# Optimization experiments

Measured on AMD Instinct MI355X. Metric: run time of the kernel, lower is better.

The kernel has to match this reference:

```python
import jax, jax.numpy as jnp
import numpy as np

CH = 256
GROUPS = 8
EPS = 1e-5


def setup_inputs() -> dict:
    key = jax.random.key(0)
    ks = jax.random.split(key, 10)
    c = CH
    s = 1.0 / np.sqrt(c)
    return {
        "x": jax.random.normal(ks[0], (4, c, 64, 64), dtype=jnp.float32),
        "gn_gamma": jnp.ones((c,), jnp.float32),
        "gn_beta": jnp.zeros((c,), jnp.float32),
        "wq": jax.random.normal(ks[1], (c, c), jnp.float32) * s,
        "bq": jnp.zeros((c,), jnp.float32),
        "wk": jax.random.normal(ks[2], (c, c), jnp.float32) * s,
        "bk": jnp.zeros((c,), jnp.float32),
        "wv": jax.random.normal(ks[3], (c, c), jnp.float32) * s,
        "bv": jnp.zeros((c,), jnp.float32),
        "wp": jax.random.normal(ks[4], (c, c), jnp.float32) * s,
        "bp": jnp.zeros((c,), jnp.float32),
    }


def group_norm(x, gamma, beta):
    b, c, h, w = x.shape
    g = GROUPS
    xg = x.reshape(b, g, c // g, h, w)
    mu = jnp.mean(xg, axis=(2, 3, 4), keepdims=True)
    var = jnp.var(xg, axis=(2, 3, 4), keepdims=True)
    xn = ((xg - mu) * jax.lax.rsqrt(var + EPS)).reshape(b, c, h, w)
    return xn * gamma[None, :, None, None] + beta[None, :, None, None]


def reference(x, gn_gamma, gn_beta, wq, bq, wk, bk, wv, bv, wp, bp):
    b, c, h, w = x.shape
    xn = group_norm(x, gn_gamma, gn_beta).reshape(b, c, h * w)  # [b,c,n]
    # 1x1 conv == channel matmul: out[b,o,n] = sum_c w[o,c] x[b,c,n] + bias
    q = jnp.einsum('oc,bcn->bon', wq, xn) + bq[None, :, None]
    k = jnp.einsum('oc,bcn->bon', wk, xn) + bk[None, :, None]
    v = jnp.einsum('oc,bcn->bon', wv, xn) + bv[None, :, None]
    scores = jnp.einsum('bcn,bcm->bnm', q, k) / jnp.sqrt(jnp.float32(c))
    attn = jax.nn.softmax(scores, axis=-1)  # [b,n,m]
    out = jnp.einsum('bnm,bcm->bcn', attn, v)
    out = jnp.einsum('oc,bcn->bon', wp, out) + bp[None, :, None]
    return out.reshape(b, c, h, w) + x
```

## Files before the change

### kernel.cpp

```cpp
#include <hip/hip_runtime.h>
#include <stdint.h>

#define BB 4
#define CC 256
#define NN 4096
#define GG 8

typedef unsigned short u16;
typedef __attribute__((ext_vector_type(4))) float f32x4;
typedef __attribute__((ext_vector_type(16))) float f32x16;
typedef __attribute__((ext_vector_type(8))) short s16x8;
typedef __attribute__((ext_vector_type(4))) u16 u16x4;
typedef __attribute__((ext_vector_type(8))) u16 u16x8;

__device__ __forceinline__ u16 f2bf(float f) {
  union { float f; uint32_t u; } v; v.f = f;
  return (u16)((v.u + 0x7FFFu + ((v.u >> 16) & 1u)) >> 16);
}
__device__ __forceinline__ float bf2f(uint32_t u) {
  union { uint32_t u; float f; } v; v.u = u << 16;
  return v.f;
}

__device__ __forceinline__ void async16(const void* g, void* l) {
  __builtin_amdgcn_global_load_lds(
      (const __attribute__((address_space(1))) void*)g,
      (__attribute__((address_space(3))) void*)l, 16, 0, 0);
}

__global__ __launch_bounds__(256) void wcvt_kernel(
    const float* __restrict__ w0, const float* __restrict__ w1,
    const float* __restrict__ w2, const float* __restrict__ w3,
    u16* __restrict__ dst) {
  const float* src = (blockIdx.y == 0) ? w0 : (blockIdx.y == 1) ? w1
                   : (blockIdx.y == 2) ? w2 : w3;
  int i = blockIdx.x * 256 + threadIdx.x;
  f32x4 v = ((const f32x4*)src)[i];
  u16x4 o;
  o[0] = f2bf(v[0]); o[1] = f2bf(v[1]); o[2] = f2bf(v[2]); o[3] = f2bf(v[3]);
  ((u16x4*)(dst + (size_t)blockIdx.y * 65536))[i] = o;
}

__global__ __launch_bounds__(256) void gn_part_kernel(
    const float* __restrict__ x, float* __restrict__ part) {
  int bg = blockIdx.x, seg = blockIdx.y;
  const f32x4* xp = (const f32x4*)(x + (size_t)bg * 131072 + seg * 16384);
  float s = 0.f, ss = 0.f;
  for (int i = threadIdx.x; i < 4096; i += 256) {
    f32x4 v = xp[i];
    s += v[0] + v[1] + v[2] + v[3];
    ss += v[0]*v[0] + v[1]*v[1] + v[2]*v[2] + v[3]*v[3];
  }
  for (int d = 1; d < 64; d <<= 1) {
    s += __shfl_xor(s, d, 64);
    ss += __shfl_xor(ss, d, 64);
  }
  __shared__ float red[8];
  int w = threadIdx.x >> 6, lane = threadIdx.x & 63;
  if (lane == 0) { red[w*2] = s; red[w*2+1] = ss; }
  __syncthreads();
  if (threadIdx.x == 0) {
    part[(bg*8 + seg)*2]     = red[0]+red[2]+red[4]+red[6];
    part[(bg*8 + seg)*2 + 1] = red[1]+red[3]+red[5]+red[7];
  }
}

__global__ __launch_bounds__(512) void gnqkv_kernel(
    const float* __restrict__ x, const float* __restrict__ part,
    const float* __restrict__ gamma, const float* __restrict__ beta,
    const u16* __restrict__ wbf,
    const float* __restrict__ bq, const float* __restrict__ bk,
    const float* __restrict__ bv,
    u16* __restrict__ Qtm, u16* __restrict__ Ktm, u16* __restrict__ Vcm) {
  __shared__ float gstat[16];
  __shared__ char t1[32768];
  __shared__ char t2[32768];
  const int b = blockIdx.y, n0 = blockIdx.x * 64, t = threadIdx.x;
  if (t < 8) {
    float S = 0.f, SS = 0.f;
    for (int seg = 0; seg < 8; ++seg) {
      S  += part[((b*8 + t)*8 + seg)*2];
      SS += part[((b*8 + t)*8 + seg)*2 + 1];
    }
    float mean = S * (1.0f/131072.0f);
    float var = SS * (1.0f/131072.0f) - mean*mean;
    gstat[t*2] = mean;
    gstat[t*2+1] = rsqrtf(var + 1e-5f);
  }
  __syncthreads();
  for (int p = 0; p < 8; ++p) {
    int c = p*32 + (t >> 4);
    int n4 = (t & 15) * 4;
    f32x4 v = *(const f32x4*)(x + ((size_t)b*CC + c)*NN + n0 + n4);
    float mean = gstat[(c>>5)*2], rstd = gstat[(c>>5)*2+1];
    float ga = gamma[c] * rstd;
    float be = beta[c] - mean * ga;
    u16x4 o;
    o[0]=f2bf(v[0]*ga+be); o[1]=f2bf(v[1]*ga+be);
    o[2]=f2bf(v[2]*ga+be); o[3]=f2bf(v[3]*ga+be);
    int swz = (((c & 7) ^ ((c >> 3) & 7)) << 4);
    *(u16x4*)(t1 + c*128 + ((n4*2) ^ swz)) = o;
  }
  __syncthreads();
  for (int p = 0; p < 4; ++p) {
    int n = p*16 + (t >> 5);
    int c0 = (t & 31) * 8;
    u16x8 o;
#pragma unroll
    for (int j = 0; j < 8; ++j) {
      int c = c0 + j;
      int swz = (((c & 7) ^ ((c >> 3) & 7)) << 4);
      o[j] = *(const u16*)(t1 + c*128 + ((n*2) ^ swz));
    }
    *(u16x8*)(t2 + n*512 + ((c0*2) ^ ((n & 7) << 4))) = o;
  }
  __syncthreads();
  const int lane = t & 63, w = t >> 6;
  const int wn = w >> 2, wo = w & 3;
  const int hi = lane >> 4, lo = lane & 15;
#pragma unroll
  for (int mat = 0; mat < 3; ++mat) {
    const u16* wm = wbf + mat*65536;
    f32x4 acc[2][4] = {};
    for (int kc = 0; kc < 8; ++kc) {
      s16x8 xf[2];
#pragma unroll
      for (int nf = 0; nf < 2; ++nf) {
        int n = wn*32 + nf*16 + lo;
        xf[nf] = *(const s16x8*)(t2 + n*512 + ((kc*64 + hi*16) ^ ((n & 7) << 4)));
      }
#pragma unroll
      for (int of = 0; of < 4; ++of) {
        int o = wo*64 + of*16 + lo;
        s16x8 wf = *(const s16x8*)(wm + (size_t)o*256 + kc*32 + hi*8);
        if (mat < 2) {
          acc[0][of] = __builtin_amdgcn_mfma_f32_16x16x32_bf16(xf[0], wf, acc[0][of], 0, 0, 0);
          acc[1][of] = __builtin_amdgcn_mfma_f32_16x16x32_bf16(xf[1], wf, acc[1][of], 0, 0, 0);
        } else {
          acc[0][of] = __builtin_amdgcn_mfma_f32_16x16x32_bf16(wf, xf[0], acc[0][of], 0, 0, 0);
          acc[1][of] = __builtin_amdgcn_mfma_f32_16x16x32_bf16(wf, xf[1], acc[1][of], 0, 0, 0);
        }
      }
    }
    if (mat < 2) {
      u16* Y = (mat == 0) ? Qtm : Ktm;
      const float* bias = (mat == 0) ? bq : bk;
#pragma unroll
      for (int nf = 0; nf < 2; ++nf)
#pragma unroll
        for (int of = 0; of < 4; ++of) {
          int oc = wo*64 + of*16 + lo;
          float bvv = bias[oc];
#pragma unroll
          for (int r = 0; r < 4; ++r) {
            int n = n0 + wn*32 + nf*16 + hi*4 + r;
            Y[((size_t)b*NN + n)*CC + oc] = f2bf(acc[nf][of][r] + bvv);
          }
        }
    } else {
#pragma unroll
      for (int nf = 0; nf < 2; ++nf)
#pragma unroll
        for (int of = 0; of < 4; ++of)
#pragma unroll
          for (int r = 0; r < 4; ++r) {
            int oc = wo*64 + of*16 + hi*4 + r;
            int n = n0 + wn*32 + nf*16 + lo;
            Vcm[((size_t)b*CC + oc)*NN + n] = f2bf(acc[nf][of][r] + bv[oc]);
          }
    }
  }
}

__global__ __launch_bounds__(256, 2) void flash_kernel(
    const u16* __restrict__ Q, const u16* __restrict__ K,
    const u16* __restrict__ V, uint32_t* __restrict__ Op32,
    float* __restrict__ Lpart) {
  __shared__ char kl[2][16384];
  __shared__ char vl[2][16384];
  const int bid = blockIdx.x;
  const int b    = bid & 3;
  const int part = ((bid >> 2) & 1) | (((bid >> 8) & 1) << 1);
  const int qb   = (bid >> 3) & 31;
  const int tid = threadIdx.x;
  const int lane = tid & 63;
  const int w = tid >> 6;
  const int cl = lane & 31;
  const int h = lane >> 5;
  const int q = qb*128 + w*32 + cl;

  s16x8 qreg[16];
  {
    const u16* qp = Q + ((size_t)b*NN + q)*CC + h*8;
#pragma unroll
    for (int kc = 0; kc < 16; ++kc) qreg[kc] = *(const s16x8*)(qp + kc*16);
  }
  f32x16 oacc[8];
#pragma unroll
  for (int i = 0; i < 8; ++i) oacc[i] = (f32x16)0.f;
  float Lp = 0.f;

  const char* kbase = (const char*)(K + (size_t)b*NN*CC);
  const char* vbase = (const char*)(V + (size_t)b*CC*NN);
  const int mbase = part*1024;

  auto stage = [&](int buf, int m0) {
#pragma unroll
    for (int p = 0; p < 4; ++p)
      async16(kbase + (size_t)(m0 + (tid & 31))*512 + ((tid >> 5) + p*8)*16,
              kl[buf] + p*4096 + tid*16);
#pragma unroll
    for (int p = 0; p < 4; ++p)
      async16(vbase + (size_t)tid*8192 + (size_t)m0*2 + p*16,
              vl[buf] + p*4096 + tid*16);
  };

  stage(0, mbase);
  stage(1, mbase + 32);

  const float SC = 0.0901684857f;

  for (int it = 0; it < 32; ++it) {
    const int cur = it & 1;
    if (it == 31) asm volatile("s_waitcnt vmcnt(0)" ::: "memory");
    else          asm volatile("s_waitcnt vmcnt(8)" ::: "memory");
    __builtin_amdgcn_s_barrier();
    asm volatile("" ::: "memory");

    f32x16 s0 = (f32x16)0.f;
    __builtin_amdgcn_s_setprio(1);
#pragma unroll
    for (int kc = 0; kc < 16; ++kc) {
      s16x8 kf = *(const s16x8*)(kl[cur] + (kc*2 + h)*512 + cl*16);
      s0 = __builtin_amdgcn_mfma_f32_32x32x16_bf16(kf, qreg[kc], s0, 0, 0, 0);
    }
    __builtin_amdgcn_s_setprio(0);

    s16x8 pf[2];
#pragma unroll
    for (int half = 0; half < 2; ++half) {
      float pe[8];
#pragma unroll
      for (int j = 0; j < 8; ++j) {
        float p = exp2f(s0[half*8 + j] * SC);
        pe[j] = p;
        Lp += p;
      }
      uint32_t a0, a1, a2, a3;
      asm("v_cvt_pk_bf16_f32 %0, %1, %2" : "=v"(a0) : "v"(pe[0]), "v"(pe[1]));
      asm("v_cvt_pk_bf16_f32 %0, %1, %2" : "=v"(a1) : "v"(pe[2]), "v"(pe[3]));
      asm("v_cvt_pk_bf16_f32 %0, %1, %2" : "=v"(a2) : "v"(pe[4]), "v"(pe[5]));
      asm("v_cvt_pk_bf16_f32 %0, %1, %2" : "=v"(a3) : "v"(pe[6]), "v"(pe[7]));
      asm("v_permlane32_swap_b32 %0, %1" : "+v"(a0), "+v"(a2));
      asm("v_permlane32_swap_b32 %0, %1" : "+v"(a1), "+v"(a3));
      union { uint32_t w[4]; s16x8 v; } u;
      u.w[0] = a0; u.w[1] = a1; u.w[2] = a2; u.w[3] = a3;
      pf[half] = u.v;
    }

    __builtin_amdgcn_s_setprio(1);
#pragma unroll
    for (int ks = 0; ks < 2; ++ks) {
#pragma unroll
      for (int ct = 0; ct < 8; ++ct) {
        s16x8 vf = *(const s16x8*)(vl[cur] + (ks*2 + h)*4096 + (ct*32 + cl)*16);
        oacc[ct] = __builtin_amdgcn_mfma_f32_32x32x16_bf16(vf, pf[ks], oacc[ct], 0, 0, 0);
      }
    }
    __builtin_amdgcn_s_setprio(0);
    __builtin_amdgcn_s_barrier();
    if (it < 30) stage(cur, mbase + (it + 2)*32);
  }

  float Lq = Lp + __shfl_xor(Lp, 32, 64);
  const int pb = part*4 + b;
  if (lane < 32) Lpart[(size_t)pb*NN + q] = Lq;
  const size_t basePB = (size_t)pb * 128 * NN;
#pragma unroll
  for (int ct = 0; ct < 8; ++ct) {
#pragma unroll
    for (int i2 = 0; i2 < 8; ++i2) {
      const int i = i2*2;
      float lo_ = oacc[ct][i], hi_ = oacc[ct][i+1];
      uint32_t pk;
      asm("v_cvt_pk_bf16_f32 %0, %1, %2" : "=v"(pk) : "v"(lo_), "v"(hi_));
      const int cp = ct*16 + ((i&3)>>1) + 4*(i>>2) + 2*h;
      Op32[basePB + (size_t)cp*NN + q] = pk;
    }
  }
}

__global__ __launch_bounds__(512) void proj_kernel(
    const uint32_t* __restrict__ Op32, const float* __restrict__ Lpart,
    const u16* __restrict__ wp, const float* __restrict__ bp,
    const float* __restrict__ resid, float* __restrict__ out) {
  __shared__ char t2[32768];
  const int b = blockIdx.y, m0 = blockIdx.x * 64, t = threadIdx.x;
  {
    const int q = m0 + (t & 63);
    const int m = t & 63;
    const int cg = t >> 6;
    float L = 0.f;
#pragma unroll
    for (int p = 0; p < 4; ++p) L += Lpart[(size_t)(p*4 + b)*NN + q];
    const float inv = 1.0f / L;
#pragma unroll
    for (int i = 0; i < 16; ++i) {
      const int cp = cg*16 + i;
      float v0 = 0.f, v1 = 0.f;
#pragma unroll
      for (int p = 0; p < 4; ++p) {
        uint32_t pk = Op32[(size_t)(p*4 + b)*128*NN + (size_t)cp*NN + q];
        v0 += bf2f(pk & 0xffffu);
        v1 += bf2f(pk >> 16);
      }
      v0 *= inv; v1 *= inv;
      uint32_t opk;
      asm("v_cvt_pk_bf16_f32 %0, %1, %2" : "=v"(opk) : "v"(v0), "v"(v1));
      *(uint32_t*)(t2 + m*512 + ((cp*4) ^ ((m & 7) << 4))) = opk;
    }
  }
  __syncthreads();
  const int lane = t & 63, w = t >> 6;
  const int wm = w >> 2, wo = w & 3;
  const int hi = lane >> 4, lo = lane & 15;
  f32x4 acc[2][4] = {};
  for (int kc = 0; kc < 8; ++kc) {
    s16x8 xf[2];
#pragma unroll
    for (int mf = 0; mf < 2; ++mf) {
      int m = wm*32 + mf*16 + lo;
      xf[mf] = *(const s16x8*)(t2 + m*512 + ((kc*64 + hi*16) ^ ((m & 7) << 4)));
    }
#pragma unroll
    for (int of = 0; of < 4; ++of) {
      int o = wo*64 + of*16 + lo;
      s16x8 wf = *(const s16x8*)(wp + (size_t)o*256 + kc*32 + hi*8);
      acc[0][of] = __builtin_amdgcn_mfma_f32_16x16x32_bf16(wf, xf[0], acc[0][of], 0, 0, 0);
      acc[1][of] = __builtin_amdgcn_mfma_f32_16x16x32_bf16(wf, xf[1], acc[1][of], 0, 0, 0);
    }
  }
#pragma unroll
  for (int mf = 0; mf < 2; ++mf)
#pragma unroll
    for (int of = 0; of < 4; ++of) {
      int oc0 = wo*64 + of*16 + hi*4;
#pragma unroll
      for (int r = 0; r < 4; ++r) {
        int m = m0 + wm*32 + mf*16 + lo;
        size_t idx = ((size_t)b*CC + oc0 + r)*NN + m;
        out[idx] = acc[mf][of][r] + bp[oc0 + r] + resid[idx];
      }
    }
}

extern "C" void kernel_launch(void* const* d_in, const int* in_sizes, int n_in,
                              void* d_out, int out_size, void* d_ws, size_t ws_size,
                              hipStream_t stream) {
  const float* x  = (const float*)d_in[0];
  const float* gg = (const float*)d_in[1];
  const float* gb = (const float*)d_in[2];
  const float* wq = (const float*)d_in[3];
  const float* bq = (const float*)d_in[4];
  const float* wk = (const float*)d_in[5];
  const float* bk = (const float*)d_in[6];
  const float* wv = (const float*)d_in[7];
  const float* bv = (const float*)d_in[8];
  const float* wp = (const float*)d_in[9];
  const float* bp = (const float*)d_in[10];
  float* out = (float*)d_out;

  char* ws = (char*)d_ws;
  const size_t MATS = (size_t)BB * NN * CC;
  u16* wbf  = (u16*)ws;
  u16* Qtm  = (u16*)(ws + (512 << 10));
  u16* Ktm  = Qtm + MATS;
  u16* Vcm  = Ktm + MATS;
  uint32_t* Op32 = (uint32_t*)(Vcm + MATS);
  float* Lpart   = (float*)(Op32 + (size_t)16*128*NN);
  float* part    = Lpart + (size_t)16*NN;

  wcvt_kernel<<<dim3(64, 4), 256, 0, stream>>>(wq, wk, wv, wp, wbf);
  gn_part_kernel<<<dim3(32, 8), 256, 0, stream>>>(x, part);
  gnqkv_kernel<<<dim3(64, 4), 512, 0, stream>>>(x, part, gg, gb, wbf,
                                                bq, bk, bv, Qtm, Ktm, Vcm);
  flash_kernel<<<512, 256, 0, stream>>>(Qtm, Ktm, Vcm, Op32, Lpart);
  proj_kernel<<<dim3(64, 4), 512, 0, stream>>>(Op32, Lpart, wbf + 3*65536,
                                               bp, x, out);
}
```

Before: 159.0 us.

## Split flash kernel waves into QK/softmax producers and PV consumers via LDS

The flash attention kernel now specializes its waves. Half compute QK^T scores and exponentials and write bf16 probabilities to a double-buffered LDS area. The other half consume them one step later for the PV MFMAs, so the two phases overlap across waves. The key split drops from four partitions to two, which halves partial outputs and the reduction work in proj_kernel. Each block covers 64 queries with dynamic LDS raised to 72KB, and exp2f is replaced with raw v_exp_f32. The larger LDS footprint may cut occupancy, and the producer/consumer barriers add sync cost per step.

```diff
diff --git a/kernel.cpp b/kernel.cpp
--- a/kernel.cpp
+++ b/kernel.cpp
@@ -176,21 +176,25 @@
     const u16* __restrict__ Q, const u16* __restrict__ K,
     const u16* __restrict__ V, uint32_t* __restrict__ Op32,
     float* __restrict__ Lpart) {
-  __shared__ char kl[2][16384];
-  __shared__ char vl[2][16384];
+  extern __shared__ char smem[];
+  char* kl = smem;
+  char* vl = smem + 32768;
+  char* pl = smem + 65536;
   const int bid = blockIdx.x;
   const int b    = bid & 3;
-  const int part = ((bid >> 2) & 1) | (((bid >> 8) & 1) << 1);
-  const int qb   = (bid >> 3) & 31;
+  const int part = (bid >> 2) & 1;
+  const int qb   = bid >> 3;
   const int tid = threadIdx.x;
   const int lane = tid & 63;
   const int w = tid >> 6;
+  const int qsub = w >> 1;
+  const int role = (w ^ (bid >> 3)) & 1;
   const int cl = lane & 31;
-  const int h = lane >> 5;
-  const int q = qb*128 + w*32 + cl;
+  const int h  = lane >> 5;
+  const int q = qb*64 + qsub*32 + cl;
 
   s16x8 qreg[16];
-  {
+  if (role == 0) {
     const u16* qp = Q + ((size_t)b*NN + q)*CC + h*8;
 #pragma unroll
     for (int kc = 0; kc < 16; ++kc) qreg[kc] = *(const s16x8*)(qp + kc*16);
@@ -200,92 +204,114 @@
   for (int i = 0; i < 8; ++i) oacc[i] = (f32x16)0.f;
   float Lp = 0.f;
 
-  const char* kbase = (const char*)(K + (size_t)b*NN*CC);
-  const char* vbase = (const char*)(V + (size_t)b*CC*NN);
-  const int mbase = part*1024;
-
-  auto stage = [&](int buf, int m0) {
+  const char* kbase = (const char*)(K + (size_t)b*NN*CC) + (size_t)part*2048*512;
+  const char* vbase = (const char*)(V + (size_t)b*CC*NN) + (size_t)part*2048*2;
+
+  auto stageK = [&](int j) {
+    char* dst = kl + (j & 1)*16384 + tid*16;
+    const char* src = kbase + (size_t)(j*32 + (tid & 31))*512 + (tid >> 5)*16;
 #pragma unroll
     for (int p = 0; p < 4; ++p)
-      async16(kbase + (size_t)(m0 + (tid & 31))*512 + ((tid >> 5) + p*8)*16,
-              kl[buf] + p*4096 + tid*16);
+      async16(src + p*128, dst + p*4096);
+  };
+  auto stageV = [&](int j) {
+    char* dst = vl + (j & 1)*16384 + tid*16;
+    const char* src = vbase + (size_t)tid*8192 + j*64;
 #pragma unroll
     for (int p = 0; p < 4; ++p)
-      async16(vbase + (size_t)tid*8192 + (size_t)m0*2 + p*16,
-              vl[buf] + p*4096 + tid*16);
+      async16(src + p*16, dst + p*4096);
   };
 
-  stage(0, mbase);
-  stage(1, mbase + 32);
+  stageK(0); stageK(1); stageV(0);
 
   const float SC = 0.0901684857f;
 
-  for (int it = 0; it < 32; ++it) {
-    const int cur = it & 1;
-    if (it == 31) asm volatile("s_waitcnt vmcnt(0)" ::: "memory");
-    else          asm volatile("s_waitcnt vmcnt(8)" ::: "memory");
+  for (int t = 0; t <= 64; ++t) {
+    if (t <= 62)      asm volatile("s_waitcnt vmcnt(8)" ::: "memory");
+    else if (t == 63) asm volatile("s_waitcnt vmcnt(4)" ::: "memory");
+    else              asm volatile("s_waitcnt vmcnt(0)" ::: "memory");
     __builtin_amdgcn_s_barrier();
     asm volatile("" ::: "memory");
 
-    f32x16 s0 = (f32x16)0.f;
-    __builtin_amdgcn_s_setprio(1);
-#pragma unroll
-    for (int kc = 0; kc < 16; ++kc) {
-      s16x8 kf = *(const s16x8*)(kl[cur] + (kc*2 + h)*512 + cl*16);
-      s0 = __builtin_amdgcn_mfma_f32_32x32x16_bf16(kf, qreg[kc], s0, 0, 0, 0);
-    }
-    __builtin_amdgcn_s_setprio(0);
-
-    s16x8 pf[2];
-#pragma unroll
-    for (int half = 0; half < 2; ++half) {
-      float pe[8];
-#pragma unroll
-      for (int j = 0; j < 8; ++j) {
-        float p = exp2f(s0[half*8 + j] * SC);
-        pe[j] = p;
-        Lp += p;
-      }
-      uint32_t a0, a1, a2, a3;
-      asm("v_cvt_pk_bf16_f32 %0, %1, %2" : "=v"(a0) : "v"(pe[0]), "v"(pe[1]));
-      asm("v_cvt_pk_bf16_f32 %0, %1, %2" : "=v"(a1) : "v"(pe[2]), "v"(pe[3]));
-      asm("v_cvt_pk_bf16_f32 %0, %1, %2" : "=v"(a2) : "v"(pe[4]), "v"(pe[5]));
-      asm("v_cvt_pk_bf16_f32 %0, %1, %2" : "=v"(a3) : "v"(pe[6]), "v"(pe[7]));
-      asm("v_permlane32_swap_b32 %0, %1" : "+v"(a0), "+v"(a2));
-      asm("v_permlane32_swap_b32 %0, %1" : "+v"(a1), "+v"(a3));
-      union { uint32_t w[4]; s16x8 v; } u;
-      u.w[0] = a0; u.w[1] = a1; u.w[2] = a2; u.w[3] = a3;
-      pf[half] = u.v;
-    }
-
-    __builtin_amdgcn_s_setprio(1);
-#pragma unroll
-    for (int ks = 0; ks < 2; ++ks) {
-#pragma unroll
-      for (int ct = 0; ct < 8; ++ct) {
-        s16x8 vf = *(const s16x8*)(vl[cur] + (ks*2 + h)*4096 + (ct*32 + cl)*16);
-        oacc[ct] = __builtin_amdgcn_mfma_f32_32x32x16_bf16(vf, pf[ks], oacc[ct], 0, 0, 0);
-      }
-    }
-    __builtin_amdgcn_s_setprio(0);
+    if (role == 0) {
+      if (t < 64) {
+        const char* kc_base = kl + (t & 1)*16384;
+        f32x16 s0 = (f32x16)0.f;
+        __builtin_amdgcn_s_setprio(1);
+#pragma unroll
+        for (int kc = 0; kc < 16; ++kc) {
+          s16x8 kf = *(const s16x8*)(kc_base + (kc*2 + h)*512 + cl*16);
+          s0 = __builtin_amdgcn_mfma_f32_32x32x16_bf16(kf, qreg[kc], s0, 0, 0, 0);
+        }
+        __builtin_amdgcn_s_setprio(0);
+        char* pw = pl + (t & 1)*4096 + qsub*2048 + h*512 + cl*16;
+#pragma unroll
+        for (int half = 0; half < 2; ++half) {
+          float pe[8];
+#pragma unroll
+          for (int j = 0; j < 8; ++j) {
+            float xs = s0[half*8 + j] * SC;
+            float p;
+            asm("v_exp_f32 %0, %1" : "=v"(p) : "v"(xs));
+            pe[j] = p;
+            Lp += p;
+          }
+          uint32_t a0, a1, a2, a3;
+          asm("v_cvt_pk_bf16_f32 %0, %1, %2" : "=v"(a0) : "v"(pe[0]), "v"(pe[1]));
+          asm("v_cvt_pk_bf16_f32 %0, %1, %2" : "=v"(a1) : "v"(pe[2]), "v"(pe[3]));
+          asm("v_cvt_pk_bf16_f32 %0, %1, %2" : "=v"(a2) : "v"(pe[4]), "v"(pe[5]));
+          asm("v_cvt_pk_bf16_f32 %0, %1, %2" : "=v"(a3) : "v"(pe[6]), "v"(pe[7]));
+          asm("v_permlane32_swap_b32 %0, %1" : "+v"(a0), "+v"(a2));
+          asm("v_permlane32_swap_b32 %0, %1" : "+v"(a1), "+v"(a3));
+          union { uint32_t wd[4]; s16x8 v; } u;
+          u.wd[0] = a0; u.wd[1] = a1; u.wd[2] = a2; u.wd[3] = a3;
+          *(s16x8*)(pw + half*1024) = u.v;
+        }
+      }
+    } else {
+      if (t > 0) {
+        const int pv = (t - 1) & 1;
+        const char* vc_base = vl + pv*16384;
+        const char* pr = pl + pv*4096 + qsub*2048 + h*512 + cl*16;
+        s16x8 pf0 = *(const s16x8*)(pr);
+        s16x8 pf1 = *(const s16x8*)(pr + 1024);
+        __builtin_amdgcn_s_setprio(1);
+#pragma unroll
+        for (int ct = 0; ct < 8; ++ct) {
+          s16x8 vf = *(const s16x8*)(vc_base + h*4096 + (ct*32 + cl)*16);
+          oacc[ct] = __builtin_amdgcn_mfma_f32_32x32x16_bf16(vf, pf0, oacc[ct], 0, 0, 0);
+        }
+#pragma unroll
+        for (int ct = 0; ct < 8; ++ct) {
+          s16x8 vf = *(const s16x8*)(vc_base + (2 + h)*4096 + (ct*32 + cl)*16);
+          oacc[ct] = __builtin_amdgcn_mfma_f32_32x32x16_bf16(vf, pf1, oacc[ct], 0, 0, 0);
+        }
+        __builtin_amdgcn_s_setprio(0);
+      }
+    }
+    asm volatile("s_waitcnt lgkmcnt(0)" ::: "memory");
     __builtin_amdgcn_s_barrier();
-    if (it < 30) stage(cur, mbase + (it + 2)*32);
-  }
-
-  float Lq = Lp + __shfl_xor(Lp, 32, 64);
+    if (t <= 61) stageK(t + 2);
+    if (t <= 62) stageV(t + 1);
+  }
+
   const int pb = part*4 + b;
-  if (lane < 32) Lpart[(size_t)pb*NN + q] = Lq;
-  const size_t basePB = (size_t)pb * 128 * NN;
-#pragma unroll
-  for (int ct = 0; ct < 8; ++ct) {
-#pragma unroll
-    for (int i2 = 0; i2 < 8; ++i2) {
-      const int i = i2*2;
-      float lo_ = oacc[ct][i], hi_ = oacc[ct][i+1];
-      uint32_t pk;
-      asm("v_cvt_pk_bf16_f32 %0, %1, %2" : "=v"(pk) : "v"(lo_), "v"(hi_));
-      const int cp = ct*16 + ((i&3)>>1) + 4*(i>>2) + 2*h;
-      Op32[basePB + (size_t)cp*NN + q] = pk;
+  if (role == 0) {
+    float Lq = Lp + __shfl_xor(Lp, 32, 64);
+    if (lane < 32) Lpart[(size_t)pb*NN + q] = Lq;
+  } else {
+    const size_t basePB = (size_t)pb * 128 * NN;
+#pragma unroll
+    for (int ct = 0; ct < 8; ++ct) {
+#pragma unroll
+      for (int i2 = 0; i2 < 8; ++i2) {
+        const int i = i2*2;
+        float lo_ = oacc[ct][i], hi_ = oacc[ct][i+1];
+        uint32_t pk;
+        asm("v_cvt_pk_bf16_f32 %0, %1, %2" : "=v"(pk) : "v"(lo_), "v"(hi_));
+        const int cp = ct*16 + ((i&3)>>1) + 4*(i>>2) + 2*h;
+        Op32[basePB + (size_t)cp*NN + q] = pk;
+      }
     }
   }
 }
@@ -302,14 +328,14 @@
     const int cg = t >> 6;
     float L = 0.f;
 #pragma unroll
-    for (int p = 0; p < 4; ++p) L += Lpart[(size_t)(p*4 + b)*NN + q];
+    for (int p = 0; p < 2; ++p) L += Lpart[(size_t)(p*4 + b)*NN + q];
     const float inv = 1.0f / L;
 #pragma unroll
     for (int i = 0; i < 16; ++i) {
       const int cp = cg*16 + i;
       float v0 = 0.f, v1 = 0.f;
 #pragma unroll
-      for (int p = 0; p < 4; ++p) {
+      for (int p = 0; p < 2; ++p) {
         uint32_t pk = Op32[(size_t)(p*4 + b)*128*NN + (size_t)cp*NN + q];
         v0 += bf2f(pk & 0xffffu);
         v1 += bf2f(pk >> 16);
@@ -377,14 +403,16 @@
   u16* Ktm  = Qtm + MATS;
   u16* Vcm  = Ktm + MATS;
   uint32_t* Op32 = (uint32_t*)(Vcm + MATS);
-  float* Lpart   = (float*)(Op32 + (size_t)16*128*NN);
-  float* part    = Lpart + (size_t)16*NN;
+  float* Lpart   = (float*)(Op32 + (size_t)8*128*NN);
+  float* part    = Lpart + (size_t)8*NN;
 
   wcvt_kernel<<<dim3(64, 4), 256, 0, stream>>>(wq, wk, wv, wp, wbf);
   gn_part_kernel<<<dim3(32, 8), 256, 0, stream>>>(x, part);
   gnqkv_kernel<<<dim3(64, 4), 512, 0, stream>>>(x, part, gg, gb, wbf,
                                                 bq, bk, bv, Qtm, Ktm, Vcm);
-  flash_kernel<<<512, 256, 0, stream>>>(Qtm, Ktm, Vcm, Op32, Lpart);
-  proj_kernel<<<dim3(64, 4), 512, 0, stream>>>(Op32, Lpart, wbf + 3*65536,
+  hipFuncSetAttribute((const void*)flash_kernel,
+                      hipFuncAttributeMaxDynamicSharedMemorySize, 73728);
+  flash_kernel<<<512, 256, 73728, stream>>>(Qtm, Ktm, Vcm, Op32, Lpart);
+  proj_kernel<<<dim3(64, 4), 512, 0, stream>>>(Op32, Lpart, wp ? wbf + 3*65536 : wbf,
                                                bp, x, out);
 }
```

Result: slower. 199.4 us (+25.4%).

## Load V fragments directly from global into registers, dropping V LDS staging

Applied to the files above, without the earlier changes.

Removes the LDS double-buffer for V and has each lane fetch its V MFMA fragments straight from global memory into registers, issued around the QK^T MFMAs so the loads overlap with that compute. The barrier and the K restage are moved earlier, right after the QK product, and the vmcnt wait is cut to match the smaller number of outstanding async loads. This halves LDS use and the LDS traffic per iteration, which may allow more blocks per CU. In exchange it relies on uncoalesced 16-byte global/L2 reads with a large stride across channels and needs more vector registers to hold the prefetched fragments.

```diff
diff --git a/kernel.cpp b/kernel.cpp
--- a/kernel.cpp
+++ b/kernel.cpp
@@ -177,7 +177,6 @@
     const u16* __restrict__ V, uint32_t* __restrict__ Op32,
     float* __restrict__ Lpart) {
   __shared__ char kl[2][16384];
-  __shared__ char vl[2][16384];
   const int bid = blockIdx.x;
   const int b    = bid & 3;
   const int part = ((bid >> 2) & 1) | (((bid >> 8) & 1) << 1);
@@ -203,29 +202,32 @@
   const char* kbase = (const char*)(K + (size_t)b*NN*CC);
   const char* vbase = (const char*)(V + (size_t)b*CC*NN);
   const int mbase = part*1024;
-
-  auto stage = [&](int buf, int m0) {
+  const char* vsrc = vbase + (size_t)mbase*2 + (size_t)cl*8192 + h*16;
+
+  auto stageK = [&](int buf, int m0) {
 #pragma unroll
     for (int p = 0; p < 4; ++p)
       async16(kbase + (size_t)(m0 + (tid & 31))*512 + ((tid >> 5) + p*8)*16,
               kl[buf] + p*4096 + tid*16);
-#pragma unroll
-    for (int p = 0; p < 4; ++p)
-      async16(vbase + (size_t)tid*8192 + (size_t)m0*2 + p*16,
-              vl[buf] + p*4096 + tid*16);
   };
 
-  stage(0, mbase);
-  stage(1, mbase + 32);
+  stageK(0, mbase);
+  stageK(1, mbase + 32);
 
   const float SC = 0.0901684857f;
 
   for (int it = 0; it < 32; ++it) {
     const int cur = it & 1;
     if (it == 31) asm volatile("s_waitcnt vmcnt(0)" ::: "memory");
-    else          asm volatile("s_waitcnt vmcnt(8)" ::: "memory");
+    else          asm volatile("s_waitcnt vmcnt(4)" ::: "memory");
     __builtin_amdgcn_s_barrier();
     asm volatile("" ::: "memory");
+
+    const char* vit = vsrc + it*64;
+    s16x8 vf0[8];
+#pragma unroll
+    for (int ct = 0; ct < 8; ++ct)
+      vf0[ct] = *(const s16x8*)(vit + (size_t)ct*262144);
 
     f32x16 s0 = (f32x16)0.f;
     __builtin_amdgcn_s_setprio(1);
@@ -235,6 +237,15 @@
       s0 = __builtin_amdgcn_mfma_f32_32x32x16_bf16(kf, qreg[kc], s0, 0, 0, 0);
     }
     __builtin_amdgcn_s_setprio(0);
+
+    s16x8 vf1[8];
+#pragma unroll
+    for (int ct = 0; ct < 8; ++ct)
+      vf1[ct] = *(const s16x8*)(vit + (size_t)ct*262144 + 32);
+
+    __builtin_amdgcn_s_barrier();
+    asm volatile("" ::: "memory");
+    if (it < 30) stageK(cur, mbase + (it + 2)*32);
 
     s16x8 pf[2];
 #pragma unroll
@@ -253,23 +264,19 @@
       asm("v_cvt_pk_bf16_f32 %0, %1, %2" : "=v"(a3) : "v"(pe[6]), "v"(pe[7]));
       asm("v_permlane32_swap_b32 %0, %1" : "+v"(a0), "+v"(a2));
       asm("v_permlane32_swap_b32 %0, %1" : "+v"(a1), "+v"(a3));
-      union { uint32_t w[4]; s16x8 v; } u;
-      u.w[0] = a0; u.w[1] = a1; u.w[2] = a2; u.w[3] = a3;
+      union { uint32_t wd[4]; s16x8 v; } u;
+      u.wd[0] = a0; u.wd[1] = a1; u.wd[2] = a2; u.wd[3] = a3;
       pf[half] = u.v;
     }
 
     __builtin_amdgcn_s_setprio(1);
 #pragma unroll
-    for (int ks = 0; ks < 2; ++ks) {
-#pragma unroll
-      for (int ct = 0; ct < 8; ++ct) {
-        s16x8 vf = *(const s16x8*)(vl[cur] + (ks*2 + h)*4096 + (ct*32 + cl)*16);
-        oacc[ct] = __builtin_amdgcn_mfma_f32_32x32x16_bf16(vf, pf[ks], oacc[ct], 0, 0, 0);
-      }
-    }
+    for (int ct = 0; ct < 8; ++ct)
+      oacc[ct] = __builtin_amdgcn_mfma_f32_32x32x16_bf16(vf0[ct], pf[0], oacc[ct], 0, 0, 0);
+#pragma unroll
+    for (int ct = 0; ct < 8; ++ct)
+      oacc[ct] = __builtin_amdgcn_mfma_f32_32x32x16_bf16(vf1[ct], pf[1], oacc[ct], 0, 0, 0);
     __builtin_amdgcn_s_setprio(0);
-    __builtin_amdgcn_s_barrier();
-    if (it < 30) stage(cur, mbase + (it + 2)*32);
   }
 
   float Lq = Lp + __shfl_xor(Lp, 32, 64);
```

Measured after the change: 424.0 us. 2.67x slower.

## Software-pipeline PV MFMA behind next QK MFMA and split GN partial stats finer

Applied to the files above, without the earlier changes.

The flash kernel loop is restructured so the P·V matmul for the previous tile runs right after the current tile's QK^T MFMAs. The softmax exponentials are then computed after the barrier and the new async loads are issued. K and V staging are split so V for the next tile loads one iteration later, with a final epilogue PV step after the loop. The aim is to overlap exp/convert VALU work with MFMA and memory latency. Separately, the group-norm partial reduction is split into 16 segments instead of 8 to launch more blocks. The change adds register pressure from keeping pf live across iterations and makes the waitcnt accounting more intricate.

```diff
diff --git a/kernel.cpp b/kernel.cpp
--- a/kernel.cpp
+++ b/kernel.cpp
@@ -44,9 +44,9 @@
 __global__ __launch_bounds__(256) void gn_part_kernel(
     const float* __restrict__ x, float* __restrict__ part) {
   int bg = blockIdx.x, seg = blockIdx.y;
-  const f32x4* xp = (const f32x4*)(x + (size_t)bg * 131072 + seg * 16384);
+  const f32x4* xp = (const f32x4*)(x + (size_t)bg * 131072 + seg * 8192);
   float s = 0.f, ss = 0.f;
-  for (int i = threadIdx.x; i < 4096; i += 256) {
+  for (int i = threadIdx.x; i < 2048; i += 256) {
     f32x4 v = xp[i];
     s += v[0] + v[1] + v[2] + v[3];
     ss += v[0]*v[0] + v[1]*v[1] + v[2]*v[2] + v[3]*v[3];
@@ -60,8 +60,8 @@
   if (lane == 0) { red[w*2] = s; red[w*2+1] = ss; }
   __syncthreads();
   if (threadIdx.x == 0) {
-    part[(bg*8 + seg)*2]     = red[0]+red[2]+red[4]+red[6];
-    part[(bg*8 + seg)*2 + 1] = red[1]+red[3]+red[5]+red[7];
+    part[(bg*16 + seg)*2]     = red[0]+red[2]+red[4]+red[6];
+    part[(bg*16 + seg)*2 + 1] = red[1]+red[3]+red[5]+red[7];
   }
 }
 
@@ -78,9 +78,9 @@
   const int b = blockIdx.y, n0 = blockIdx.x * 64, t = threadIdx.x;
   if (t < 8) {
     float S = 0.f, SS = 0.f;
-    for (int seg = 0; seg < 8; ++seg) {
-      S  += part[((b*8 + t)*8 + seg)*2];
-      SS += part[((b*8 + t)*8 + seg)*2 + 1];
+    for (int seg = 0; seg < 16; ++seg) {
+      S  += part[((b*8 + t)*16 + seg)*2];
+      SS += part[((b*8 + t)*16 + seg)*2 + 1];
     }
     float mean = S * (1.0f/131072.0f);
     float var = SS * (1.0f/131072.0f) - mean*mean;
@@ -204,25 +204,29 @@
   const char* vbase = (const char*)(V + (size_t)b*CC*NN);
   const int mbase = part*1024;
 
-  auto stage = [&](int buf, int m0) {
+  auto stageK = [&](int buf, int m0) {
 #pragma unroll
     for (int p = 0; p < 4; ++p)
       async16(kbase + (size_t)(m0 + (tid & 31))*512 + ((tid >> 5) + p*8)*16,
               kl[buf] + p*4096 + tid*16);
+  };
+  auto stageV = [&](int buf, int m0) {
 #pragma unroll
     for (int p = 0; p < 4; ++p)
       async16(vbase + (size_t)tid*8192 + (size_t)m0*2 + p*16,
               vl[buf] + p*4096 + tid*16);
   };
 
-  stage(0, mbase);
-  stage(1, mbase + 32);
+  stageK(0, mbase);
+  stageK(1, mbase + 32);
+  stageV(0, mbase);
 
   const float SC = 0.0901684857f;
+  s16x8 pf[2];
 
   for (int it = 0; it < 32; ++it) {
     const int cur = it & 1;
-    if (it == 31) asm volatile("s_waitcnt vmcnt(0)" ::: "memory");
+    if (it == 31) asm volatile("s_waitcnt vmcnt(4)" ::: "memory");
     else          asm volatile("s_waitcnt vmcnt(8)" ::: "memory");
     __builtin_amdgcn_s_barrier();
     asm volatile("" ::: "memory");
@@ -234,9 +238,23 @@
       s16x8 kf = *(const s16x8*)(kl[cur] + (kc*2 + h)*512 + cl*16);
       s0 = __builtin_amdgcn_mfma_f32_32x32x16_bf16(kf, qreg[kc], s0, 0, 0, 0);
     }
+    if (it > 0) {
+      const char* vc = vl[cur ^ 1];
+#pragma unroll
+      for (int ks = 0; ks < 2; ++ks) {
+#pragma unroll
+        for (int ct = 0; ct < 8; ++ct) {
+          s16x8 vf = *(const s16x8*)(vc + (ks*2 + h)*4096 + (ct*32 + cl)*16);
+          oacc[ct] = __builtin_amdgcn_mfma_f32_32x32x16_bf16(vf, pf[ks], oacc[ct], 0, 0, 0);
+        }
+      }
+    }
     __builtin_amdgcn_s_setprio(0);
-
-    s16x8 pf[2];
+    __builtin_amdgcn_s_barrier();
+    asm volatile("" ::: "memory");
+    if (it < 30) stageK(cur, mbase + (it + 2)*32);
+    if (it < 31) stageV(cur ^ 1, mbase + (it + 1)*32);
+
 #pragma unroll
     for (int half = 0; half < 2; ++half) {
       float pe[8];
@@ -253,23 +271,27 @@
       asm("v_cvt_pk_bf16_f32 %0, %1, %2" : "=v"(a3) : "v"(pe[6]), "v"(pe[7]));
       asm("v_permlane32_swap_b32 %0, %1" : "+v"(a0), "+v"(a2));
       asm("v_permlane32_swap_b32 %0, %1" : "+v"(a1), "+v"(a3));
-      union { uint32_t w[4]; s16x8 v; } u;
-      u.w[0] = a0; u.w[1] = a1; u.w[2] = a2; u.w[3] = a3;
+      union { uint32_t wd[4]; s16x8 v; } u;
+      u.wd[0] = a0; u.wd[1] = a1; u.wd[2] = a2; u.wd[3] = a3;
       pf[half] = u.v;
     }
-
+  }
+
+  asm volatile("s_waitcnt vmcnt(0)" ::: "memory");
+  __builtin_amdgcn_s_barrier();
+  asm volatile("" ::: "memory");
+  {
+    const char* vc = vl[1];
     __builtin_amdgcn_s_setprio(1);
 #pragma unroll
     for (int ks = 0; ks < 2; ++ks) {
 #pragma unroll
       for (int ct = 0; ct < 8; ++ct) {
-        s16x8 vf = *(const s16x8*)(vl[cur] + (ks*2 + h)*4096 + (ct*32 + cl)*16);
+        s16x8 vf = *(const s16x8*)(vc + (ks*2 + h)*4096 + (ct*32 + cl)*16);
         oacc[ct] = __builtin_amdgcn_mfma_f32_32x32x16_bf16(vf, pf[ks], oacc[ct], 0, 0, 0);
       }
     }
     __builtin_amdgcn_s_setprio(0);
-    __builtin_amdgcn_s_barrier();
-    if (it < 30) stage(cur, mbase + (it + 2)*32);
   }
 
   float Lq = Lp + __shfl_xor(Lp, 32, 64);
@@ -381,7 +403,7 @@
   float* part    = Lpart + (size_t)16*NN;
 
   wcvt_kernel<<<dim3(64, 4), 256, 0, stream>>>(wq, wk, wv, wp, wbf);
-  gn_part_kernel<<<dim3(32, 8), 256, 0, stream>>>(x, part);
+  gn_part_kernel<<<dim3(32, 16), 256, 0, stream>>>(x, part);
   gnqkv_kernel<<<dim3(64, 4), 512, 0, stream>>>(x, part, gg, gb, wbf,
                                                 bq, bk, bv, Qtm, Ktm, Vcm);
   flash_kernel<<<512, 256, 0, stream>>>(Qtm, Ktm, Vcm, Op32, Lpart);
```

Result: faster. 153.5 us (-3.5%).
